# Kernel optimization log

Hardware: AMD Instinct MI355X
Metric: run time of the kernel (lower is better)

Reference implementation:

```python
import jax, jax.numpy as jnp
import numpy as np

ALPHA = 0.5
WIN_SIZE = 31
BN_EPS = 1e-5
LRELU_SLOPE = 0.1


def setup_inputs() -> dict:
    key = jax.random.key(0)
    k1, k2, k3, k4 = jax.random.split(key, 4)
    B, N, C, P, E = 4, 2048, 64, 48, 128
    return {
        "sig_new": jax.random.normal(k1, (B, N, C, P), dtype=jnp.float32),
        "atten_mem": jax.random.normal(k2, (B, N, C, P), dtype=jnp.float32),
        "conv_w": jax.random.normal(k3, (E, C, P), dtype=jnp.float32) * 0.05,
        "conv_b": jax.random.normal(k4, (E,), dtype=jnp.float32) * 0.05,
        "bn_gamma": jnp.ones((E,), dtype=jnp.float32),
        "bn_beta": jnp.zeros((E,), dtype=jnp.float32),
    }


def _neighbour_mask(n_cutout):
    # clamped banded mask (pano_scan=False / training-mode branch)
    half = WIN_SIZE // 2
    cols = jnp.clip(jnp.arange(n_cutout)[:, None] + jnp.arange(-half, half + 1)[None, :], 0, n_cutout - 1)
    rows = jnp.broadcast_to(jnp.arange(n_cutout)[:, None], cols.shape)
    return jnp.zeros((n_cutout, n_cutout), jnp.float32).at[rows, cols].set(1.0)


def _embed(x, conv_w, conv_b, bn_gamma, bn_beta, B, N):
    # Conv1d(kernel=n_pts) on length-n_pts input == full contraction over (c, p)
    y = jnp.einsum("ncp,ecp->ne", x.reshape(-1, x.shape[-2], x.shape[-1]), conv_w) + conv_b
    # BatchNorm1d, training-mode batch statistics over the (B*N) batch dim
    mu = y.mean(axis=0)
    var = ((y - mu) ** 2).mean(axis=0)
    y = (y - mu) * jax.lax.rsqrt(var + BN_EPS) * bn_gamma + bn_beta
    y = jnp.where(y >= 0, y, LRELU_SLOPE * y)  # LeakyReLU(0.1)
    return y.reshape(B, N, -1)


def reference(sig_new, atten_mem, conv_w, conv_b, bn_gamma, bn_beta):
    B, N, C, P = sig_new.shape
    mask = _neighbour_mask(N)
    embed_x = _embed(sig_new, conv_w, conv_b, bn_gamma, bn_beta, B, N)      # [B,N,E]
    embed_t = _embed(atten_mem, conv_w, conv_b, bn_gamma, bn_beta, B, N)    # [B,N,E]
    sim = jnp.einsum("bie,bje->bij", embed_x, embed_t)                      # [B,N,N]
    sim = sim - 1e10 * (1.0 - mask)
    mx = jnp.max(sim, axis=-1, keepdims=True)
    ex = jnp.exp(sim - mx) * mask
    attn = ex / jnp.sum(ex, axis=-1, keepdims=True)                          # [B,N,N]
    mem_flat = atten_mem.reshape(B, N, C * P)
    mem_w = jnp.einsum("bij,bjf->bif", attn, mem_flat).reshape(B, N, C, P)
    new_mem = ALPHA * sig_new + (1.0 - ALPHA) * mem_w
    return new_mem, attn
```

## Files before the change

kernel.cpp:

```cpp
#include <hip/hip_runtime.h>

#define BATCH 4
#define NDIM 2048
#define EDIM 128
#define KDIM 3072
#define MDIM 8192
#define HALF 15

#define BM 64
#define BK 32
#define LDA_S 72
#define LDW_S 136

__global__ __launch_bounds__(256, 2)
void k_gemm(const float* __restrict__ x0, const float* __restrict__ x1,
            const float* __restrict__ w, float* __restrict__ part, int splitK) {
  const int tid = threadIdx.x;
  const int m0 = blockIdx.x * BM;
  const int kc = blockIdx.y;
  const int inp = blockIdx.z;
  const float* __restrict__ x = inp ? x1 : x0;
  const int kpc = KDIM / splitK;
  const int kbeg = kc * kpc;
  const int kend = kbeg + kpc;

  __shared__ float sA[BK][LDA_S];
  __shared__ float sW[BK][LDW_S];

  const int lr = tid >> 3;
  const int lk = (tid & 7) << 2;
  const int mg = tid >> 4;
  const int eg = tid & 15;

  float acc[4][8];
#pragma unroll
  for (int a = 0; a < 4; ++a)
#pragma unroll
    for (int q = 0; q < 8; ++q) acc[a][q] = 0.f;

  float4 ra0, ra1, rw0, rw1, rw2, rw3;
  {
    const float* xb = x + (size_t)(m0 + lr) * KDIM + kbeg + lk;
    ra0 = *(const float4*)xb;
    ra1 = *(const float4*)(xb + (size_t)32 * KDIM);
    const float* wb = w + (size_t)lr * KDIM + kbeg + lk;
    rw0 = *(const float4*)wb;
    rw1 = *(const float4*)(wb + (size_t)32 * KDIM);
    rw2 = *(const float4*)(wb + (size_t)64 * KDIM);
    rw3 = *(const float4*)(wb + (size_t)96 * KDIM);
  }

  for (int kt = kbeg; kt < kend; kt += BK) {
    __syncthreads();
#pragma unroll
    for (int j = 0; j < 4; ++j) {
      sA[lk + j][lr]      = ((const float*)&ra0)[j];
      sA[lk + j][lr + 32] = ((const float*)&ra1)[j];
      sW[lk + j][lr]      = ((const float*)&rw0)[j];
      sW[lk + j][lr + 32] = ((const float*)&rw1)[j];
      sW[lk + j][lr + 64] = ((const float*)&rw2)[j];
      sW[lk + j][lr + 96] = ((const float*)&rw3)[j];
    }
    __syncthreads();
    if (kt + BK < kend) {
      const float* xb = x + (size_t)(m0 + lr) * KDIM + (kt + BK) + lk;
      ra0 = *(const float4*)xb;
      ra1 = *(const float4*)(xb + (size_t)32 * KDIM);
      const float* wb = w + (size_t)lr * KDIM + (kt + BK) + lk;
      rw0 = *(const float4*)wb;
      rw1 = *(const float4*)(wb + (size_t)32 * KDIM);
      rw2 = *(const float4*)(wb + (size_t)64 * KDIM);
      rw3 = *(const float4*)(wb + (size_t)96 * KDIM);
    }
#pragma unroll
    for (int k = 0; k < BK; ++k) {
      float4 a4 = *(const float4*)&sA[k][mg << 2];
      float4 b0 = *(const float4*)&sW[k][eg << 3];
      float4 b1 = *(const float4*)&sW[k][(eg << 3) + 4];
      const float av[4] = {a4.x, a4.y, a4.z, a4.w};
      const float bv[8] = {b0.x, b0.y, b0.z, b0.w, b1.x, b1.y, b1.z, b1.w};
#pragma unroll
      for (int mi = 0; mi < 4; ++mi)
#pragma unroll
        for (int ei = 0; ei < 8; ++ei)
          acc[mi][ei] = fmaf(av[mi], bv[ei], acc[mi][ei]);
    }
  }

  float* po = part + ((size_t)(inp * splitK + kc) * MDIM + (m0 + (mg << 2))) * EDIM + (eg << 3);
#pragma unroll
  for (int mi = 0; mi < 4; ++mi) {
    float4 o0 = {acc[mi][0], acc[mi][1], acc[mi][2], acc[mi][3]};
    float4 o1 = {acc[mi][4], acc[mi][5], acc[mi][6], acc[mi][7]};
    *(float4*)(po + (size_t)mi * EDIM) = o0;
    *(float4*)(po + (size_t)mi * EDIM + 4) = o1;
  }
}

__global__ __launch_bounds__(256)
void k_reduce(const float* __restrict__ part, const float* __restrict__ bvec,
              float* __restrict__ y, float* __restrict__ spart, int splitK) {
  const int tid = threadIdx.x;
  const int in = blockIdx.z;
  const int rb = blockIdx.x;
  const int e = tid & 127;
  const int rh = tid >> 7;
  const float bb = bvec[e];
  float s = 0.f, s2 = 0.f;
  for (int rr = 0; rr < 32; ++rr) {
    const int r = rb * 64 + rh * 32 + rr;
    float v = 0.f;
    for (int kc = 0; kc < splitK; ++kc)
      v += part[((size_t)(in * splitK + kc) * MDIM + r) * EDIM + e];
    v += bb;
    y[((size_t)in * MDIM + r) * EDIM + e] = v;
    s += v; s2 += v * v;
  }
  __shared__ float l1[256], l2[256];
  l1[tid] = s; l2[tid] = s2;
  __syncthreads();
  if (rh == 0) {
    s = l1[e] + l1[e + 128];
    s2 = l2[e] + l2[e + 128];
    spart[((size_t)(in * 128 + rb) * 2 + 0) * 128 + e] = s;
    spart[((size_t)(in * 128 + rb) * 2 + 1) * 128 + e] = s2;
  }
}

__global__ void k_finalize(const float* __restrict__ spart, const float* __restrict__ gamma,
                           const float* __restrict__ beta, float* __restrict__ scsh) {
  const int in = blockIdx.x;
  const int e = threadIdx.x;
  float s = 0.f, s2 = 0.f;
  for (int rb = 0; rb < 128; ++rb) {
    s  += spart[((size_t)(in * 128 + rb) * 2 + 0) * 128 + e];
    s2 += spart[((size_t)(in * 128 + rb) * 2 + 1) * 128 + e];
  }
  const float mu = s * (1.f / MDIM);
  const float var = s2 * (1.f / MDIM) - mu * mu;
  const float rs = rsqrtf(var + 1e-5f);
  const float sc = gamma[e] * rs;
  const float sh = beta[e] - mu * sc;
  scsh[in * 128 + e] = sc;
  scsh[256 + in * 128 + e] = sh;
}

__global__ __launch_bounds__(256)
void k_bnapply(float* __restrict__ y, const float* __restrict__ scsh) {
  int q = blockIdx.x * 256 + threadIdx.x;
  float4* yv = (float4*)y;
#pragma unroll
  for (int it = 0; it < 2; ++it, q += 262144) {
    float4 v = yv[q];
    const int in = q >> 18;
    const int e0 = (q & 31) << 2;
    const float* sc = scsh + in * 128 + e0;
    const float* sh = scsh + 256 + in * 128 + e0;
    float t;
    t = fmaf(sc[0], v.x, sh[0]); v.x = t >= 0.f ? t : 0.1f * t;
    t = fmaf(sc[1], v.y, sh[1]); v.y = t >= 0.f ? t : 0.1f * t;
    t = fmaf(sc[2], v.z, sh[2]); v.z = t >= 0.f ? t : 0.1f * t;
    t = fmaf(sc[3], v.w, sh[3]); v.w = t >= 0.f ? t : 0.1f * t;
    yv[q] = v;
  }
}

__global__ __launch_bounds__(256)
void k_sim(const float* __restrict__ y, float* __restrict__ attn, float* __restrict__ aw) {
  const int tid = threadIdx.x;
  const int row = blockIdx.x * 4 + (tid >> 6);
  const int lane = tid & 63;
  const int b = row >> 11;
  const int i = row & 2047;
  const int jlo = max(0, i - HALF);
  const int jhi = min(NDIM - 1, i + HALF);
  const int j = jlo + lane;
  const bool valid = (lane < 31) && (j <= jhi);
  const int jc = valid ? j : jlo;
  const float* __restrict__ xr = y + (size_t)row * EDIM;
  const float* __restrict__ tr = y + (size_t)MDIM * EDIM + ((size_t)(b << 11) + jc) * EDIM;
  float s = 0.f;
#pragma unroll
  for (int e = 0; e < EDIM; e += 4) {
    float4 u = *(const float4*)(xr + e);
    float4 v = *(const float4*)(tr + e);
    s = fmaf(u.x, v.x, s); s = fmaf(u.y, v.y, s);
    s = fmaf(u.z, v.z, s); s = fmaf(u.w, v.w, s);
  }
  float sm = valid ? s : -1e30f;
  float mx = sm;
#pragma unroll
  for (int o = 1; o < 64; o <<= 1) mx = fmaxf(mx, __shfl_xor(mx, o));
  const float p = valid ? __expf(sm - mx) : 0.f;
  float ss = p;
#pragma unroll
  for (int o = 1; o < 64; o <<= 1) ss += __shfl_xor(ss, o);
  const float a = p / ss;
  if (valid) attn[(size_t)row * NDIM + j] = a;
  if (lane < 32) aw[(size_t)row * 32 + lane] = valid ? a : 0.f;
}

#define TI 16
#define TJMAX 46
#define FC 256

__global__ __launch_bounds__(256, 2)
void k_memw(const float* __restrict__ sig, const float* __restrict__ mem,
            const float* __restrict__ aw, float* __restrict__ out) {
  const int tid = threadIdx.x;
  const int fc0 = blockIdx.x * FC;
  const int i0 = blockIdx.y * TI;
  const int b = blockIdx.z;
  const int jlo = max(0, i0 - HALF);
  const int jhi = min(NDIM - 1, i0 + TI - 1 + HALF);
  const int tj = jhi - jlo + 1;

  __shared__ float sV[TJMAX][FC];
  __shared__ float sWt[TJMAX][TI];

  for (int idx = tid; idx < tj * TI; idx += 256) {
    const int jj = idx >> 4;
    const int ii = idx & 15;
    const int ii_g = i0 + ii;
    const int jg = jlo + jj;
    const int jli = max(0, ii_g - HALF);
    const int jhii = min(NDIM - 1, ii_g + HALF);
    float wv = 0.f;
    if (jg >= jli && jg <= jhii) wv = aw[(size_t)((b << 11) + ii_g) * 32 + (jg - jli)];
    sWt[jj][ii] = wv;
  }
  for (int idx = tid; idx < tj * (FC / 4); idx += 256) {
    const int jj = idx >> 6;
    const int f4 = idx & 63;
    *(float4*)&sV[jj][f4 << 2] =
        *(const float4*)(mem + (size_t)((b << 11) + jlo + jj) * KDIM + fc0 + (f4 << 2));
  }
  __syncthreads();

  const int ig = tid >> 6;
  const int fg = tid & 63;
  const int ibase = i0 + (ig << 2);
  const int wlo = max(jlo, ibase - HALF) - jlo;
  const int whi = min(jhi, ibase + 3 + HALF) - jlo;

  float acc[4][4];
#pragma unroll
  for (int a = 0; a < 4; ++a)
#pragma unroll
    for (int c = 0; c < 4; ++c) acc[a][c] = 0.f;

  for (int jj = wlo; jj <= whi; ++jj) {
    float4 wv = *(const float4*)&sWt[jj][ig << 2];
    float4 vv = *(const float4*)&sV[jj][fg << 2];
    const float wa[4] = {wv.x, wv.y, wv.z, wv.w};
    const float va[4] = {vv.x, vv.y, vv.z, vv.w};
#pragma unroll
    for (int mi = 0; mi < 4; ++mi)
#pragma unroll
      for (int fi = 0; fi < 4; ++fi)
        acc[mi][fi] = fmaf(wa[mi], va[fi], acc[mi][fi]);
  }

  const size_t base = (size_t)((b << 11) + ibase) * KDIM + fc0 + (fg << 2);
#pragma unroll
  for (int mi = 0; mi < 4; ++mi) {
    float4 sv = *(const float4*)(sig + base + (size_t)mi * KDIM);
    float4 ov;
    ov.x = 0.5f * sv.x + 0.5f * acc[mi][0];
    ov.y = 0.5f * sv.y + 0.5f * acc[mi][1];
    ov.z = 0.5f * sv.z + 0.5f * acc[mi][2];
    ov.w = 0.5f * sv.w + 0.5f * acc[mi][3];
    *(float4*)(out + base + (size_t)mi * KDIM) = ov;
  }
}

extern "C" void kernel_launch(void* const* d_in, const int* in_sizes, int n_in,
                              void* d_out, int out_size, void* d_ws, size_t ws_size,
                              hipStream_t stream) {
  const float* sig   = (const float*)d_in[0];
  const float* mem   = (const float*)d_in[1];
  const float* w     = (const float*)d_in[2];
  const float* bv    = (const float*)d_in[3];
  const float* gamma = (const float*)d_in[4];
  const float* beta  = (const float*)d_in[5];

  float* out_mem  = (float*)d_out;
  float* out_attn = out_mem + (size_t)BATCH * NDIM * KDIM;

  float* wsf = (float*)d_ws;
  const size_t ME = (size_t)MDIM * EDIM;
  const size_t fixed = 2 * ME + 65536 + 512 + 262144;
  int splitK = 4;
  while (splitK > 1 && ((size_t)2 * splitK * ME + fixed) * 4 > ws_size) splitK >>= 1;

  float* part  = wsf;
  float* y     = part + (size_t)2 * splitK * ME;
  float* spart = y + 2 * ME;
  float* scsh  = spart + 65536;
  float* aw    = scsh + 512;

  hipMemsetAsync(out_attn, 0, (size_t)BATCH * NDIM * NDIM * sizeof(float), stream);

  dim3 g1(MDIM / BM, splitK, 2);
  hipLaunchKernelGGL(k_gemm, g1, dim3(256), 0, stream, sig, mem, w, part, splitK);

  dim3 g2(MDIM / 64, 1, 2);
  hipLaunchKernelGGL(k_reduce, g2, dim3(256), 0, stream, part, bv, y, spart, splitK);

  hipLaunchKernelGGL(k_finalize, dim3(2), dim3(128), 0, stream, spart, gamma, beta, scsh);

  hipLaunchKernelGGL(k_bnapply, dim3(1024), dim3(256), 0, stream, y, scsh);

  hipLaunchKernelGGL(k_sim, dim3(MDIM / 4), dim3(256), 0, stream, y, out_attn, aw);

  dim3 g6(KDIM / FC, NDIM / TI, BATCH);
  hipLaunchKernelGGL(k_memw, g6, dim3(256), 0, stream, sig, mem, aw, out_mem);
}
```

Before: 571.5 us.

## Use split-bf16 MFMA (3-term) for the embedding GEMM instead of FP32 FMA

```diff
diff --git a/kernel.cpp b/kernel.cpp
--- a/kernel.cpp
+++ b/kernel.cpp
@@ -7,93 +7,133 @@
 #define MDIM 8192
 #define HALF 15
 
-#define BM 64
+typedef __attribute__((ext_vector_type(8))) short short8v;
+typedef __attribute__((ext_vector_type(4))) float f32x4;
+
+__device__ inline ushort bf16h(float x) {
+  union { float f; unsigned u; } v; v.f = x;
+  unsigned r = v.u + 0x7fff + ((v.u >> 16) & 1);
+  return (ushort)(r >> 16);
+}
+__device__ inline float bf2f(ushort h) {
+  union { unsigned u; float f; } v; v.u = ((unsigned)h) << 16;
+  return v.f;
+}
+
+#define BMT 128
 #define BK 32
-#define LDA_S 72
-#define LDW_S 136
 
 __global__ __launch_bounds__(256, 2)
 void k_gemm(const float* __restrict__ x0, const float* __restrict__ x1,
             const float* __restrict__ w, float* __restrict__ part, int splitK) {
   const int tid = threadIdx.x;
-  const int m0 = blockIdx.x * BM;
+  const int m0 = blockIdx.x * BMT;
   const int kc = blockIdx.y;
   const int inp = blockIdx.z;
   const float* __restrict__ x = inp ? x1 : x0;
   const int kpc = KDIM / splitK;
   const int kbeg = kc * kpc;
-  const int kend = kbeg + kpc;
-
-  __shared__ float sA[BK][LDA_S];
-  __shared__ float sW[BK][LDW_S];
-
-  const int lr = tid >> 3;
-  const int lk = (tid & 7) << 2;
-  const int mg = tid >> 4;
-  const int eg = tid & 15;
-
-  float acc[4][8];
+  const int nsteps = kpc / BK;
+
+  __shared__ ushort sAh[BMT][BK];
+  __shared__ ushort sAl[BMT][BK];
+  __shared__ ushort sBh[EDIM][BK];
+  __shared__ ushort sBl[EDIM][BK];
+
+  const int mrow = tid >> 3;
+  const int c4 = (tid & 7) << 2;
+
+  const int lane = tid & 63;
+  const int wid = tid >> 6;
+  const int wr = wid >> 1;
+  const int wc = wid & 1;
+  const int fr = lane & 15;
+  const int kg = (lane >> 4) << 3;
+
+  f32x4 acc[4][4];
 #pragma unroll
   for (int a = 0; a < 4; ++a)
 #pragma unroll
-    for (int q = 0; q < 8; ++q) acc[a][q] = 0.f;
-
-  float4 ra0, ra1, rw0, rw1, rw2, rw3;
+    for (int b = 0; b < 4; ++b) acc[a][b] = (f32x4){0.f, 0.f, 0.f, 0.f};
+
+  float4 rA[4], rB[4];
   {
-    const float* xb = x + (size_t)(m0 + lr) * KDIM + kbeg + lk;
-    ra0 = *(const float4*)xb;
-    ra1 = *(const float4*)(xb + (size_t)32 * KDIM);
-    const float* wb = w + (size_t)lr * KDIM + kbeg + lk;
-    rw0 = *(const float4*)wb;
-    rw1 = *(const float4*)(wb + (size_t)32 * KDIM);
-    rw2 = *(const float4*)(wb + (size_t)64 * KDIM);
-    rw3 = *(const float4*)(wb + (size_t)96 * KDIM);
-  }
-
-  for (int kt = kbeg; kt < kend; kt += BK) {
+    const float* xb = x + (size_t)(m0 + mrow) * KDIM + kbeg + c4;
+    const float* wb = w + (size_t)mrow * KDIM + kbeg + c4;
+#pragma unroll
+    for (int i = 0; i < 4; ++i) {
+      rA[i] = *(const float4*)(xb + (size_t)(32 * i) * KDIM);
+      rB[i] = *(const float4*)(wb + (size_t)(32 * i) * KDIM);
+    }
+  }
+
+  for (int st = 0; st < nsteps; ++st) {
     __syncthreads();
 #pragma unroll
-    for (int j = 0; j < 4; ++j) {
-      sA[lk + j][lr]      = ((const float*)&ra0)[j];
-      sA[lk + j][lr + 32] = ((const float*)&ra1)[j];
-      sW[lk + j][lr]      = ((const float*)&rw0)[j];
-      sW[lk + j][lr + 32] = ((const float*)&rw1)[j];
-      sW[lk + j][lr + 64] = ((const float*)&rw2)[j];
-      sW[lk + j][lr + 96] = ((const float*)&rw3)[j];
+    for (int i = 0; i < 4; ++i) {
+      const int m = mrow + 32 * i;
+      const float fa[4] = {rA[i].x, rA[i].y, rA[i].z, rA[i].w};
+      const float fb[4] = {rB[i].x, rB[i].y, rB[i].z, rB[i].w};
+      ushort4 ah, al, bh, bl;
+      ushort* pah = (ushort*)&ah; ushort* pal = (ushort*)&al;
+      ushort* pbh = (ushort*)&bh; ushort* pbl = (ushort*)&bl;
+#pragma unroll
+      for (int j = 0; j < 4; ++j) {
+        ushort h = bf16h(fa[j]); pah[j] = h; pal[j] = bf16h(fa[j] - bf2f(h));
+        ushort g = bf16h(fb[j]); pbh[j] = g; pbl[j] = bf16h(fb[j] - bf2f(g));
+      }
+      *(ushort4*)&sAh[m][c4] = ah;
+      *(ushort4*)&sAl[m][c4] = al;
+      *(ushort4*)&sBh[m][c4] = bh;
+      *(ushort4*)&sBl[m][c4] = bl;
     }
     __syncthreads();
-    if (kt + BK < kend) {
-      const float* xb = x + (size_t)(m0 + lr) * KDIM + (kt + BK) + lk;
-      ra0 = *(const float4*)xb;
-      ra1 = *(const float4*)(xb + (size_t)32 * KDIM);
-      const float* wb = w + (size_t)lr * KDIM + (kt + BK) + lk;
-      rw0 = *(const float4*)wb;
-      rw1 = *(const float4*)(wb + (size_t)32 * KDIM);
-      rw2 = *(const float4*)(wb + (size_t)64 * KDIM);
-      rw3 = *(const float4*)(wb + (size_t)96 * KDIM);
-    }
-#pragma unroll
-    for (int k = 0; k < BK; ++k) {
-      float4 a4 = *(const float4*)&sA[k][mg << 2];
-      float4 b0 = *(const float4*)&sW[k][eg << 3];
-      float4 b1 = *(const float4*)&sW[k][(eg << 3) + 4];
-      const float av[4] = {a4.x, a4.y, a4.z, a4.w};
-      const float bv[8] = {b0.x, b0.y, b0.z, b0.w, b1.x, b1.y, b1.z, b1.w};
-#pragma unroll
-      for (int mi = 0; mi < 4; ++mi)
-#pragma unroll
-        for (int ei = 0; ei < 8; ++ei)
-          acc[mi][ei] = fmaf(av[mi], bv[ei], acc[mi][ei]);
-    }
-  }
-
-  float* po = part + ((size_t)(inp * splitK + kc) * MDIM + (m0 + (mg << 2))) * EDIM + (eg << 3);
+
+    if (st + 1 < nsteps) {
+      const int ko = kbeg + (st + 1) * BK + c4;
+      const float* xb = x + (size_t)(m0 + mrow) * KDIM + ko;
+      const float* wb = w + (size_t)mrow * KDIM + ko;
+#pragma unroll
+      for (int i = 0; i < 4; ++i) {
+        rA[i] = *(const float4*)(xb + (size_t)(32 * i) * KDIM);
+        rB[i] = *(const float4*)(wb + (size_t)(32 * i) * KDIM);
+      }
+    }
+
+    short8v ah[4], al[4], bh[4], bl[4];
+#pragma unroll
+    for (int mi = 0; mi < 4; ++mi) {
+      const int row = wr * 64 + mi * 16 + fr;
+      ah[mi] = *(const short8v*)&sAh[row][kg];
+      al[mi] = *(const short8v*)&sAl[row][kg];
+    }
+#pragma unroll
+    for (int ei = 0; ei < 4; ++ei) {
+      const int e = wc * 64 + ei * 16 + fr;
+      bh[ei] = *(const short8v*)&sBh[e][kg];
+      bl[ei] = *(const short8v*)&sBl[e][kg];
+    }
+#pragma unroll
+    for (int mi = 0; mi < 4; ++mi)
+#pragma unroll
+      for (int ei = 0; ei < 4; ++ei) {
+        acc[mi][ei] = __builtin_amdgcn_mfma_f32_16x16x32_bf16(ah[mi], bh[ei], acc[mi][ei], 0, 0, 0);
+        acc[mi][ei] = __builtin_amdgcn_mfma_f32_16x16x32_bf16(ah[mi], bl[ei], acc[mi][ei], 0, 0, 0);
+        acc[mi][ei] = __builtin_amdgcn_mfma_f32_16x16x32_bf16(al[mi], bh[ei], acc[mi][ei], 0, 0, 0);
+      }
+  }
+
+  float* po = part + ((size_t)(inp * splitK + kc) * MDIM + m0) * EDIM;
 #pragma unroll
   for (int mi = 0; mi < 4; ++mi) {
-    float4 o0 = {acc[mi][0], acc[mi][1], acc[mi][2], acc[mi][3]};
-    float4 o1 = {acc[mi][4], acc[mi][5], acc[mi][6], acc[mi][7]};
-    *(float4*)(po + (size_t)mi * EDIM) = o0;
-    *(float4*)(po + (size_t)mi * EDIM + 4) = o1;
+    const int mloc = wr * 64 + mi * 16 + ((lane >> 4) << 2);
+#pragma unroll
+    for (int ei = 0; ei < 4; ++ei) {
+      const int e = wc * 64 + ei * 16 + fr;
+#pragma unroll
+      for (int r = 0; r < 4; ++r)
+        po[(size_t)(mloc + r) * EDIM + e] = acc[mi][ei][r];
+    }
   }
 }
 
@@ -301,7 +341,7 @@
 
   hipMemsetAsync(out_attn, 0, (size_t)BATCH * NDIM * NDIM * sizeof(float), stream);
 
-  dim3 g1(MDIM / BM, splitK, 2);
+  dim3 g1(MDIM / BMT, splitK, 2);
   hipLaunchKernelGGL(k_gemm, g1, dim3(256), 0, stream, sig, mem, w, part, splitK);
 
   dim3 g2(MDIM / 64, 1, 2);
```

Result: faster. 475.0 us (-16.9%).
